# Kernel tuning notes

Hardware: AMD Instinct MI355X
Metric: run time of the kernel (lower is better)

## Reference

```python
import jax, jax.numpy as jnp
import numpy as np

EPS = 0.3
LAYER_NUM = 2
N_NODES = 50000
N_EDGES = 1600000
IN_CH = 256
HIDDEN = 128
OUT_CH = 64


def setup_inputs() -> dict:
    key = jax.random.key(0)
    ks = jax.random.split(key, 8)
    x = jax.random.normal(ks[0], (N_NODES, IN_CH), dtype=jnp.float32)
    edge_index = jax.random.randint(ks[1], (2, N_EDGES), 0, N_NODES, dtype=jnp.int64)
    # xavier-normal-ish scales
    t1_w = jax.random.normal(ks[2], (HIDDEN, IN_CH), dtype=jnp.float32) * (1.414 * (2.0 / (IN_CH + HIDDEN)) ** 0.5)
    t1_b = jnp.zeros((HIDDEN,), dtype=jnp.float32)
    gate_w = jax.random.normal(ks[3], (LAYER_NUM, 2 * HIDDEN), dtype=jnp.float32) * ((2.0 / (2 * HIDDEN + 1)) ** 0.5)
    gate_b = jnp.zeros((LAYER_NUM,), dtype=jnp.float32)
    t2_w = jax.random.normal(ks[4], (OUT_CH, HIDDEN), dtype=jnp.float32) * (1.414 * (2.0 / (HIDDEN + OUT_CH)) ** 0.5)
    t2_b = jnp.zeros((OUT_CH,), dtype=jnp.float32)
    return {"x": x, "edge_index": edge_index, "t1_w": t1_w, "t1_b": t1_b,
            "gate_w": gate_w, "gate_b": gate_b, "t2_w": t2_w, "t2_b": t2_b}


def reference(x, edge_index, t1_w, t1_b, gate_w, gate_b, t2_w, t2_b):
    n = x.shape[0]
    row, col = edge_index[0], edge_index[1]
    # symmetric degree normalization: deg computed over target nodes (row)
    deg = jax.ops.segment_sum(jnp.ones_like(row, dtype=x.dtype), row, num_segments=n)
    dinv = jnp.where(deg > 0, jax.lax.rsqrt(jnp.maximum(deg, 1.0)), 0.0)  # [N]
    edge_norm = dinv[row] * dinv[col]  # [E]

    h = jax.nn.relu(x @ t1_w.T + t1_b)  # [N, H]
    raw = h
    H = h.shape[1]
    for l in range(LAYER_NUM):
        gw_i = gate_w[l, :H]   # weights for h_src (row)
        gw_j = gate_w[l, H:]   # weights for h_dst (col)
        # edge attention g = tanh(gate([h_row || h_col]))  -> [E]
        g = jnp.tanh(h[row] @ gw_i + h[col] @ gw_j + gate_b[l])
        w = g * edge_norm  # [E]
        # scatter-add weighted neighbor features to target nodes
        agg = jax.ops.segment_sum(w[:, None] * h[col], row, num_segments=n)  # [N, H]
        h = EPS * raw + agg
    out = h @ t2_w.T + t2_b  # [N, out]
    return jax.nn.log_softmax(out, axis=1)
```

## Files before the change

### kernel.cpp

```cpp
#include <hip/hip_runtime.h>
#include <math.h>

#define EPSF 0.3f
#define NPB 128
#define SHB 7
#define MAXNB 512
#define CHUNK 4096

typedef __attribute__((ext_vector_type(8))) short bf16x8;
typedef __attribute__((ext_vector_type(4))) float f32x4;

__device__ __forceinline__ uint32_t f2bf(float f) {
    uint32_t u = __float_as_uint(f);
    return (u + 0x7fffu + ((u >> 16) & 1u)) >> 16;
}
__device__ __forceinline__ uint32_t pack2(float lo, float hi) {
    return f2bf(lo) | (f2bf(hi) << 16);
}
__device__ __forceinline__ float bflo(uint32_t u) { return __uint_as_float(u << 16); }
__device__ __forceinline__ float bfhi(uint32_t u) { return __uint_as_float(u & 0xffff0000u); }

__device__ __forceinline__ float fast_tanh(float x) {
    float e = __expf(2.f * x);
    return 1.f - 2.f * __builtin_amdgcn_rcpf(e + 1.f);
}

__device__ __forceinline__ int edge_at(const int* ei, int is64, size_t idx) {
    if (is64) return (int)((const long long*)ei)[idx];
    return ei[idx];
}

__device__ __forceinline__ int detect_is64(const int* ei, int base, int E) {
    __shared__ int s_nz;
    if (threadIdx.x == 0) s_nz = 0;
    __syncthreads();
    int lim = min(512, E - base);
    int nz = 0;
    for (int t = threadIdx.x; t < lim; t += 256)
        nz |= (ei[2 * (size_t)(base + t) + 1] != 0);
    if (nz) atomicOr(&s_nz, 1);
    __syncthreads();
    return s_nz == 0;
}

__global__ __launch_bounds__(256) void k_hist(const int* __restrict__ ei, int E,
                                              int* __restrict__ hist, int nblk, int NB) {
    __shared__ int lh[MAXNB];
    int base = blockIdx.x * CHUNK;
    int is64 = detect_is64(ei, base, E);
    for (int b = threadIdx.x; b < NB; b += 256) lh[b] = 0;
    __syncthreads();
    for (int j = threadIdx.x; j < CHUNK; j += 256) {
        int e = base + j;
        if (e < E) {
            int r = edge_at(ei, is64, e);
            atomicAdd(&lh[r >> SHB], 1);
        }
    }
    __syncthreads();
    for (int b = threadIdx.x; b < NB; b += 256)
        hist[(size_t)b * nblk + blockIdx.x] = lh[b];
}

__global__ void k_scanA(int* __restrict__ hist, int nblk, int* __restrict__ btot) {
    int b = blockIdx.x;
    int lane = threadIdx.x;
    int run = 0;
    for (int seg = 0; seg < nblk; seg += 64) {
        int idx = seg + lane;
        int v = (idx < nblk) ? hist[(size_t)b * nblk + idx] : 0;
        int s = v;
        for (int o = 1; o < 64; o <<= 1) {
            int t = __shfl_up(s, o);
            if (lane >= o) s += t;
        }
        if (idx < nblk) hist[(size_t)b * nblk + idx] = run + s - v;
        run += __shfl(s, 63);
    }
    if (lane == 0) btot[b] = run;
}

__global__ void k_scanB(const int* __restrict__ btot, int NB, int* __restrict__ bbase) {
    __shared__ int s[MAXNB];
    int t = threadIdx.x;
    int v = (t < NB) ? btot[t] : 0;
    s[t] = v;
    __syncthreads();
    for (int o = 1; o < MAXNB; o <<= 1) {
        int x = (t >= o) ? s[t - o] : 0;
        __syncthreads();
        s[t] += x;
        __syncthreads();
    }
    if (t < NB) bbase[t] = s[t] - v;
    if (t == MAXNB - 1) bbase[NB] = s[t];
}

__global__ __launch_bounds__(256) void k_binwrite(const int* __restrict__ ei, int E,
                                                  const int* __restrict__ hist,
                                                  const int* __restrict__ bbase,
                                                  uint32_t* __restrict__ ebuf,
                                                  int nblk, int NB) {
    __shared__ int lcnt[MAXNB];
    int base = blockIdx.x * CHUNK;
    int is64 = detect_is64(ei, base, E);
    for (int b = threadIdx.x; b < NB; b += 256)
        lcnt[b] = bbase[b] + hist[(size_t)b * nblk + blockIdx.x];
    __syncthreads();
    for (int j = threadIdx.x; j < CHUNK; j += 256) {
        int e = base + j;
        if (e < E) {
            int r = edge_at(ei, is64, e);
            int c = edge_at(ei, is64, (size_t)E + e);
            int pos = atomicAdd(&lcnt[r >> SHB], 1);
            ebuf[pos] = (uint32_t)(r & (NPB - 1)) | ((uint32_t)c << SHB);
        }
    }
}

__global__ __launch_bounds__(256) void k_csr(const uint32_t* __restrict__ ebuf,
                                             const int* __restrict__ bbase,
                                             int* __restrict__ rp, float* __restrict__ dinv,
                                             int* __restrict__ ecol, int N, int E, int NB) {
    __shared__ int cnt[NPB];
    __shared__ int sc[NPB];
    __shared__ int cur[NPB];
    int b = blockIdx.x;
    int tid = threadIdx.x;
    int p0 = bbase[b], p1 = bbase[b + 1];
    int n0 = b << SHB;
    if (tid < NPB) cnt[tid] = 0;
    __syncthreads();
    for (int p = p0 + tid; p < p1; p += 256)
        atomicAdd(&cnt[ebuf[p] & (NPB - 1)], 1);
    __syncthreads();
    if (tid < NPB) sc[tid] = cnt[tid];
    __syncthreads();
    for (int o = 1; o < NPB; o <<= 1) {
        int v = (tid < NPB && tid >= o) ? sc[tid - o] : 0;
        __syncthreads();
        if (tid < NPB) sc[tid] += v;
        __syncthreads();
    }
    if (tid < NPB) {
        int off = sc[tid] - cnt[tid];
        cur[tid] = off;
        int node = n0 + tid;
        if (node < N) {
            rp[node] = p0 + off;
            int d = cnt[tid];
            dinv[node] = d > 0 ? rsqrtf((float)d) : 0.f;
        }
    }
    if (b == NB - 1 && tid == 0) rp[N] = E;
    __syncthreads();
    for (int p = p0 + tid; p < p1; p += 256) {
        uint32_t v = ebuf[p];
        int pos = p0 + atomicAdd(&cur[v & (NPB - 1)], 1);
        ecol[pos] = (int)(v >> SHB);
    }
}

__global__ __launch_bounds__(256) void k_gemm1(const float* __restrict__ A,
                                               const float* __restrict__ W,
                                               const float* __restrict__ bias,
                                               uint32_t* __restrict__ hb, int M) {
    __shared__ char As[128 * 128];
    __shared__ char Bs[128 * 128];
    const int tid = threadIdx.x;
    const int lane = tid & 63;
    const int wave = tid >> 6;
    const int wr = wave >> 1, wc = wave & 1;
    const int m0 = blockIdx.x * 128;
    const int lrow = lane & 15, lkg = lane >> 4;
    const int sr = tid >> 3;
    const int sc = (tid & 7) * 8;

    f32x4 acc[4][4];
#pragma unroll
    for (int mi = 0; mi < 4; ++mi)
#pragma unroll
        for (int ni = 0; ni < 4; ++ni) acc[mi][ni] = (f32x4){0.f, 0.f, 0.f, 0.f};

    for (int t = 0; t < 4; ++t) {
        const int k0 = t * 64;
#pragma unroll
        for (int i = 0; i < 4; ++i) {
            int r = i * 32 + sr;
            float4 v0 = make_float4(0.f, 0.f, 0.f, 0.f), v1 = v0;
            if (m0 + r < M) {
                const float* p = &A[(size_t)(m0 + r) * 256 + k0 + sc];
                v0 = *(const float4*)p;
                v1 = *(const float4*)(p + 4);
            }
            uint4 pk = make_uint4(pack2(v0.x, v0.y), pack2(v0.z, v0.w),
                                  pack2(v1.x, v1.y), pack2(v1.z, v1.w));
            uint32_t off = (uint32_t)(r * 128 + sc * 2);
            *(uint4*)(As + (off ^ ((r & 7) << 4))) = pk;
        }
#pragma unroll
        for (int i = 0; i < 4; ++i) {
            int r = i * 32 + sr;
            const float* p = &W[(size_t)r * 256 + k0 + sc];
            float4 v0 = *(const float4*)p;
            float4 v1 = *(const float4*)(p + 4);
            uint4 pk = make_uint4(pack2(v0.x, v0.y), pack2(v0.z, v0.w),
                                  pack2(v1.x, v1.y), pack2(v1.z, v1.w));
            uint32_t off = (uint32_t)(r * 128 + sc * 2);
            *(uint4*)(Bs + (off ^ ((r & 7) << 4))) = pk;
        }
        __syncthreads();
#pragma unroll
        for (int ks = 0; ks < 2; ++ks) {
            bf16x8 af[4], bfr[4];
#pragma unroll
            for (int mi = 0; mi < 4; ++mi) {
                int r = wr * 64 + mi * 16 + lrow;
                uint32_t off = (uint32_t)(r * 128 + ks * 64 + lkg * 16);
                af[mi] = *(const bf16x8*)(As + (off ^ ((r & 7) << 4)));
            }
#pragma unroll
            for (int ni = 0; ni < 4; ++ni) {
                int r = wc * 64 + ni * 16 + lrow;
                uint32_t off = (uint32_t)(r * 128 + ks * 64 + lkg * 16);
                bfr[ni] = *(const bf16x8*)(Bs + (off ^ ((r & 7) << 4)));
            }
#pragma unroll
            for (int mi = 0; mi < 4; ++mi)
#pragma unroll
                for (int ni = 0; ni < 4; ++ni)
                    acc[mi][ni] = __builtin_amdgcn_mfma_f32_16x16x32_bf16(
                        af[mi], bfr[ni], acc[mi][ni], 0, 0, 0);
        }
        __syncthreads();
    }
#pragma unroll
    for (int mi = 0; mi < 4; ++mi) {
#pragma unroll
        for (int ni = 0; ni < 4; ++ni) {
            int n = wc * 64 + ni * 16 + lrow;
            float bv = bias[n];
#pragma unroll
            for (int q = 0; q < 4; ++q) {
                float v = fmaxf(acc[mi][ni][q] + bv, 0.f);
                float vp = __shfl_xor(v, 1);
                int m = m0 + wr * 64 + mi * 16 + lkg * 4 + q;
                if (!(lane & 1) && m < M)
                    hb[(size_t)m * 64 + (n >> 1)] = pack2(v, vp);
            }
        }
    }
}

__global__ __launch_bounds__(256) void k_gemm2(const uint32_t* __restrict__ Abf,
                                               const float* __restrict__ W,
                                               const float* __restrict__ bias,
                                               float* __restrict__ out, int M) {
    __shared__ char As[128 * 128];
    __shared__ char Bs[64 * 128];
    __shared__ float redmax[2][128];
    __shared__ float redsum[2][128];
    const int tid = threadIdx.x;
    const int lane = tid & 63;
    const int wave = tid >> 6;
    const int wr = wave >> 1, wc = wave & 1;
    const int m0 = blockIdx.x * 128;
    const int lrow = lane & 15, lkg = lane >> 4;

    f32x4 acc[4][2];
#pragma unroll
    for (int mi = 0; mi < 4; ++mi)
#pragma unroll
        for (int ni = 0; ni < 2; ++ni) acc[mi][ni] = (f32x4){0.f, 0.f, 0.f, 0.f};

    for (int t = 0; t < 2; ++t) {
#pragma unroll
        for (int i = 0; i < 4; ++i) {
            int r = i * 32 + (tid >> 3);
            uint4 v = make_uint4(0u, 0u, 0u, 0u);
            if (m0 + r < M)
                v = *(const uint4*)&Abf[(size_t)(m0 + r) * 64 + t * 32 + (tid & 7) * 4];
            uint32_t off = (uint32_t)(r * 128 + (tid & 7) * 16);
            *(uint4*)(As + (off ^ ((r & 7) << 4))) = v;
        }
#pragma unroll
        for (int i = 0; i < 2; ++i) {
            int r = i * 32 + (tid >> 3);
            const float* p = &W[(size_t)r * 128 + t * 64 + (tid & 7) * 8];
            float4 v0 = *(const float4*)p, v1 = *(const float4*)(p + 4);
            uint4 pk = make_uint4(pack2(v0.x, v0.y), pack2(v0.z, v0.w),
                                  pack2(v1.x, v1.y), pack2(v1.z, v1.w));
            uint32_t off = (uint32_t)(r * 128 + (tid & 7) * 16);
            *(uint4*)(Bs + (off ^ ((r & 7) << 4))) = pk;
        }
        __syncthreads();
#pragma unroll
        for (int ks = 0; ks < 2; ++ks) {
            bf16x8 af[4], bfr[2];
#pragma unroll
            for (int mi = 0; mi < 4; ++mi) {
                int r = wr * 64 + mi * 16 + lrow;
                uint32_t off = (uint32_t)(r * 128 + ks * 64 + lkg * 16);
                af[mi] = *(const bf16x8*)(As + (off ^ ((r & 7) << 4)));
            }
#pragma unroll
            for (int ni = 0; ni < 2; ++ni) {
                int r = wc * 32 + ni * 16 + lrow;
                uint32_t off = (uint32_t)(r * 128 + ks * 64 + lkg * 16);
                bfr[ni] = *(const bf16x8*)(Bs + (off ^ ((r & 7) << 4)));
            }
#pragma unroll
            for (int mi = 0; mi < 4; ++mi)
#pragma unroll
                for (int ni = 0; ni < 2; ++ni)
                    acc[mi][ni] = __builtin_amdgcn_mfma_f32_16x16x32_bf16(
                        af[mi], bfr[ni], acc[mi][ni], 0, 0, 0);
        }
        __syncthreads();
    }

    float vb[4][2][4];
#pragma unroll
    for (int mi = 0; mi < 4; ++mi)
#pragma unroll
        for (int ni = 0; ni < 2; ++ni) {
            float bv = bias[wc * 32 + ni * 16 + lrow];
#pragma unroll
            for (int q = 0; q < 4; ++q) vb[mi][ni][q] = acc[mi][ni][q] + bv;
        }
#pragma unroll
    for (int mi = 0; mi < 4; ++mi)
#pragma unroll
        for (int q = 0; q < 4; ++q) {
            float mx = fmaxf(vb[mi][0][q], vb[mi][1][q]);
#pragma unroll
            for (int o = 1; o < 16; o <<= 1) mx = fmaxf(mx, __shfl_xor(mx, o));
            if (lrow == 0) redmax[wc][wr * 64 + mi * 16 + lkg * 4 + q] = mx;
        }
    __syncthreads();
    float fmv[4][4];
#pragma unroll
    for (int mi = 0; mi < 4; ++mi)
#pragma unroll
        for (int q = 0; q < 4; ++q) {
            int rl = wr * 64 + mi * 16 + lkg * 4 + q;
            float fm = fmaxf(redmax[0][rl], redmax[1][rl]);
            fmv[mi][q] = fm;
            float e = expf(vb[mi][0][q] - fm) + expf(vb[mi][1][q] - fm);
#pragma unroll
            for (int o = 1; o < 16; o <<= 1) e += __shfl_xor(e, o);
            if (lrow == 0) redsum[wc][rl] = e;
        }
    __syncthreads();
#pragma unroll
    for (int mi = 0; mi < 4; ++mi)
#pragma unroll
        for (int q = 0; q < 4; ++q) {
            int rl = wr * 64 + mi * 16 + lkg * 4 + q;
            int m = m0 + rl;
            if (m < M) {
                float ls = logf(redsum[0][rl] + redsum[1][rl]) + fmv[mi][q];
                out[(size_t)m * 64 + wc * 32 + lrow] = vb[mi][0][q] - ls;
                out[(size_t)m * 64 + wc * 32 + 16 + lrow] = vb[mi][1][q] - ls;
            }
        }
}

__global__ void k_ab(const uint32_t* __restrict__ hbv, const float* __restrict__ gw,
                     const float* __restrict__ gb, int layer,
                     const float* __restrict__ dinv,
                     float* __restrict__ av, float2* __restrict__ bd, int N) {
    int wid = threadIdx.x >> 6, lane = threadIdx.x & 63;
    int i = blockIdx.x * 4 + wid;
    if (i >= N) return;
    uint32_t u = hbv[(size_t)i * 64 + lane];
    float hx = bflo(u), hy = bfhi(u);
    float2 wi = *(const float2*)&gw[lane * 2];
    float2 wj = *(const float2*)&gw[128 + lane * 2];
    float pa = hx * wi.x + hy * wi.y;
    float pb = hx * wj.x + hy * wj.y;
    for (int o = 1; o < 64; o <<= 1) {
        pa += __shfl_xor(pa, o);
        pb += __shfl_xor(pb, o);
    }
    if (lane == 0) {
        av[i] = pa + gb[layer];
        bd[i] = make_float2(pb, dinv[i]);
    }
}

template <bool FUSE_AB, bool RAW_NT>
__global__ __launch_bounds__(256) void k_agg(const uint32_t* __restrict__ hb,
                                             const uint32_t* __restrict__ raw,
                                             const int* __restrict__ rp,
                                             const int* __restrict__ ecol,
                                             const float* __restrict__ av,
                                             const float2* __restrict__ bd,
                                             const float* __restrict__ dinv,
                                             uint32_t* __restrict__ hb_out,
                                             const float* __restrict__ gw_next,
                                             const float* __restrict__ gb_next,
                                             float* __restrict__ av_out,
                                             float2* __restrict__ bd_out, int N) {
    int wid = threadIdx.x >> 6, lane = threadIdx.x & 63;
    int i = blockIdx.x * 4 + wid;
    if (i >= N) return;
    int iu = __builtin_amdgcn_readfirstlane(i);
    int p0 = __builtin_amdgcn_readfirstlane(rp[iu]);
    int p1 = __builtin_amdgcn_readfirstlane(rp[iu + 1]);
    float a_i = av[iu];
    float di = dinv[iu];
    const int lg = lane >> 4;
    const int ll = lane & 15;

    uint32_t r0 = 0, r1 = 0, r2 = 0, r3 = 0;
    if (lane < 16) {
        const uint32_t* rpt = raw + (size_t)i * 64 + ll * 4;
        if (RAW_NT) {
            r0 = __builtin_nontemporal_load(rpt + 0);
            r1 = __builtin_nontemporal_load(rpt + 1);
            r2 = __builtin_nontemporal_load(rpt + 2);
            r3 = __builtin_nontemporal_load(rpt + 3);
        } else {
            r0 = rpt[0]; r1 = rpt[1]; r2 = rpt[2]; r3 = rpt[3];
        }
    }

    float acc[8];
#pragma unroll
    for (int j = 0; j < 8; ++j) acc[j] = 0.f;

    for (int b0 = p0; b0 < p1; b0 += 64) {
        int cnt = min(64, p1 - b0);
        uint32_t wcp = 0u;
        if (lane < cnt) {
            int c = __builtin_nontemporal_load(&ecol[b0 + lane]);
            float2 t = bd[c];
            float w = fast_tanh(a_i + t.x) * t.y;
            wcp = (f2bf(w) << 16) | (uint32_t)c;
        }
        int k = 0;
        for (; k + 8 <= cnt; k += 8) {
            uint32_t wx0 = __builtin_amdgcn_ds_bpermute((k + lg) << 2, (int)wcp);
            uint32_t wx1 = __builtin_amdgcn_ds_bpermute((k + 4 + lg) << 2, (int)wcp);
            float w0 = bfhi(wx0);
            float w1 = bfhi(wx1);
            int c0 = (int)(wx0 & 0xffffu);
            int c1 = (int)(wx1 & 0xffffu);
            uint4 u0 = *((const uint4*)(hb + ((size_t)c0 << 6)) + ll);
            uint4 u1 = *((const uint4*)(hb + ((size_t)c1 << 6)) + ll);
            acc[0] = fmaf(w0, bflo(u0.x), acc[0]); acc[1] = fmaf(w0, bfhi(u0.x), acc[1]);
            acc[2] = fmaf(w0, bflo(u0.y), acc[2]); acc[3] = fmaf(w0, bfhi(u0.y), acc[3]);
            acc[4] = fmaf(w0, bflo(u0.z), acc[4]); acc[5] = fmaf(w0, bfhi(u0.z), acc[5]);
            acc[6] = fmaf(w0, bflo(u0.w), acc[6]); acc[7] = fmaf(w0, bfhi(u0.w), acc[7]);
            acc[0] = fmaf(w1, bflo(u1.x), acc[0]); acc[1] = fmaf(w1, bfhi(u1.x), acc[1]);
            acc[2] = fmaf(w1, bflo(u1.y), acc[2]); acc[3] = fmaf(w1, bfhi(u1.y), acc[3]);
            acc[4] = fmaf(w1, bflo(u1.z), acc[4]); acc[5] = fmaf(w1, bfhi(u1.z), acc[5]);
            acc[6] = fmaf(w1, bflo(u1.w), acc[6]); acc[7] = fmaf(w1, bfhi(u1.w), acc[7]);
        }
        for (; k < cnt; k += 4) {
            uint32_t wx = __builtin_amdgcn_ds_bpermute((k + lg) << 2, (int)wcp);
            float w = bfhi(wx);
            int c = (int)(wx & 0xffffu);
            uint4 u = *((const uint4*)(hb + ((size_t)c << 6)) + ll);
            acc[0] = fmaf(w, bflo(u.x), acc[0]); acc[1] = fmaf(w, bfhi(u.x), acc[1]);
            acc[2] = fmaf(w, bflo(u.y), acc[2]); acc[3] = fmaf(w, bfhi(u.y), acc[3]);
            acc[4] = fmaf(w, bflo(u.z), acc[4]); acc[5] = fmaf(w, bfhi(u.z), acc[5]);
            acc[6] = fmaf(w, bflo(u.w), acc[6]); acc[7] = fmaf(w, bfhi(u.w), acc[7]);
        }
    }
#pragma unroll
    for (int j = 0; j < 8; ++j) {
        acc[j] += __shfl_xor(acc[j], 16);
        acc[j] += __shfl_xor(acc[j], 32);
    }
    if (lane < 16) {
        float o[8];
        o[0] = EPSF * bflo(r0) + di * acc[0]; o[1] = EPSF * bfhi(r0) + di * acc[1];
        o[2] = EPSF * bflo(r1) + di * acc[2]; o[3] = EPSF * bfhi(r1) + di * acc[3];
        o[4] = EPSF * bflo(r2) + di * acc[4]; o[5] = EPSF * bfhi(r2) + di * acc[5];
        o[6] = EPSF * bflo(r3) + di * acc[6]; o[7] = EPSF * bfhi(r3) + di * acc[7];
        uint4 w4;
        w4.x = pack2(o[0], o[1]); w4.y = pack2(o[2], o[3]);
        w4.z = pack2(o[4], o[5]); w4.w = pack2(o[6], o[7]);
        *((uint4*)(hb_out + (size_t)i * 64) + ll) = w4;
        if (FUSE_AB) {
            float pa = 0.f, pb = 0.f;
#pragma unroll
            for (int j = 0; j < 8; ++j) {
                int ch = ll * 8 + j;
                pa = fmaf(o[j], gw_next[ch], pa);
                pb = fmaf(o[j], gw_next[128 + ch], pb);
            }
#pragma unroll
            for (int off = 1; off < 16; off <<= 1) {
                pa += __shfl_xor(pa, off);
                pb += __shfl_xor(pb, off);
            }
            if (ll == 0) {
                av_out[i] = pa + gb_next[0];
                bd_out[i] = make_float2(pb, di);
            }
        }
    }
}

extern "C" void kernel_launch(void* const* d_in, const int* in_sizes, int n_in,
                              void* d_out, int out_size, void* d_ws, size_t ws_size,
                              hipStream_t stream) {
    const float* x = (const float*)d_in[0];
    const int* ei = (const int*)d_in[1];
    const float* t1w = (const float*)d_in[2];
    const float* t1b = (const float*)d_in[3];
    const float* gw = (const float*)d_in[4];
    const float* gb = (const float*)d_in[5];
    const float* t2w = (const float*)d_in[6];
    const float* t2b = (const float*)d_in[7];
    float* out = (float*)d_out;

    const int INC = 256;
    const int N = in_sizes[0] / INC;
    const int E = in_sizes[1] / 2;
    const int NB = (N + NPB - 1) >> SHB;
    const int nblk = (E + CHUNK - 1) / CHUNK;

    char* ws = (char*)d_ws;
    auto alloc = [&](size_t bytes) {
        char* p = ws;
        ws += (bytes + 255) & ~(size_t)255;
        return p;
    };
    int* hist = (int*)alloc((size_t)NB * nblk * 4);
    int* btot = (int*)alloc((size_t)NB * 4);
    int* bbase = (int*)alloc((size_t)(NB + 1) * 4);
    uint32_t* ebuf = (uint32_t*)alloc((size_t)E * 4);
    int* rp = (int*)alloc((size_t)(N + 1) * 4);
    float* dinv = (float*)alloc((size_t)N * 4);
    int* ecol = (int*)alloc((size_t)E * 4);
    float* av0 = (float*)alloc((size_t)N * 4);
    float* av1 = (float*)alloc((size_t)N * 4);
    float2* bd0 = (float2*)alloc((size_t)N * 8);
    float2* bd1 = (float2*)alloc((size_t)N * 8);
    uint32_t* hb0 = (uint32_t*)alloc((size_t)N * 64 * 4);
    uint32_t* hb1 = (uint32_t*)alloc((size_t)N * 64 * 4);
    uint32_t* hb2 = (uint32_t*)alloc((size_t)N * 64 * 4);

    k_hist<<<nblk, 256, 0, stream>>>(ei, E, hist, nblk, NB);
    k_scanA<<<NB, 64, 0, stream>>>(hist, nblk, btot);
    k_scanB<<<1, MAXNB, 0, stream>>>(btot, NB, bbase);
    k_binwrite<<<nblk, 256, 0, stream>>>(ei, E, hist, bbase, ebuf, nblk, NB);
    k_csr<<<NB, 256, 0, stream>>>(ebuf, bbase, rp, dinv, ecol, N, E, NB);

    k_gemm1<<<(N + 127) / 128, 256, 0, stream>>>(x, t1w, t1b, hb0, N);

    k_ab<<<(N + 3) / 4, 256, 0, stream>>>(hb0, gw + 0 * 256, gb, 0, dinv, av0, bd0, N);
    k_agg<true, false><<<(N + 3) / 4, 256, 0, stream>>>(
        hb0, hb0, rp, ecol, av0, bd0, dinv, hb1, gw + 1 * 256, gb + 1, av1, bd1, N);
    k_agg<false, true><<<(N + 3) / 4, 256, 0, stream>>>(
        hb1, hb0, rp, ecol, av1, bd1, dinv, hb2, nullptr, nullptr, nullptr, nullptr, N);

    k_gemm2<<<(N + 127) / 128, 256, 0, stream>>>(hb2, t2w, t2b, out, N);
}
```

Before: 205.1 us.

## Bin edges by row block and column range to improve gather locality

The counting-sort key becomes (row block, column bucket of 8192 nodes) instead of row block alone, so edges inside each CSR row block end up grouped by source-column range. This aims to make the later neighbor feature gathers more cache-local. In exchange the histogram grows (NB*NCB keys per chunk, about 2.3k with the default sizes), scanA becomes a serial per-key loop over chunks, and scanB becomes a single-block multi-pass scan. Both add preprocessing cost.

Measured after the change: 313.1 us. 1.53x slower.

```diff
diff --git a/kernel.cpp b/kernel.cpp
--- a/kernel.cpp
+++ b/kernel.cpp
@@ -4,7 +4,8 @@
 #define EPSF 0.3f
 #define NPB 128
 #define SHB 7
-#define MAXNB 512
+#define CBSH 13
+#define MAXK 4096
 #define CHUNK 4096
 
 typedef __attribute__((ext_vector_type(8))) short bf16x8;
@@ -44,75 +45,82 @@
 }
 
 __global__ __launch_bounds__(256) void k_hist(const int* __restrict__ ei, int E,
-                                              int* __restrict__ hist, int nblk, int NB) {
-    __shared__ int lh[MAXNB];
+                                              int* __restrict__ hist, int nkeys, int NCB) {
+    __shared__ int lh[MAXK];
     int base = blockIdx.x * CHUNK;
     int is64 = detect_is64(ei, base, E);
-    for (int b = threadIdx.x; b < NB; b += 256) lh[b] = 0;
-    __syncthreads();
-    for (int j = threadIdx.x; j < CHUNK; j += 256) {
-        int e = base + j;
-        if (e < E) {
-            int r = edge_at(ei, is64, e);
-            atomicAdd(&lh[r >> SHB], 1);
-        }
-    }
-    __syncthreads();
-    for (int b = threadIdx.x; b < NB; b += 256)
-        hist[(size_t)b * nblk + blockIdx.x] = lh[b];
-}
-
-__global__ void k_scanA(int* __restrict__ hist, int nblk, int* __restrict__ btot) {
-    int b = blockIdx.x;
-    int lane = threadIdx.x;
-    int run = 0;
-    for (int seg = 0; seg < nblk; seg += 64) {
-        int idx = seg + lane;
-        int v = (idx < nblk) ? hist[(size_t)b * nblk + idx] : 0;
-        int s = v;
-        for (int o = 1; o < 64; o <<= 1) {
-            int t = __shfl_up(s, o);
-            if (lane >= o) s += t;
-        }
-        if (idx < nblk) hist[(size_t)b * nblk + idx] = run + s - v;
-        run += __shfl(s, 63);
-    }
-    if (lane == 0) btot[b] = run;
-}
-
-__global__ void k_scanB(const int* __restrict__ btot, int NB, int* __restrict__ bbase) {
-    __shared__ int s[MAXNB];
-    int t = threadIdx.x;
-    int v = (t < NB) ? btot[t] : 0;
-    s[t] = v;
-    __syncthreads();
-    for (int o = 1; o < MAXNB; o <<= 1) {
-        int x = (t >= o) ? s[t - o] : 0;
-        __syncthreads();
-        s[t] += x;
-        __syncthreads();
-    }
-    if (t < NB) bbase[t] = s[t] - v;
-    if (t == MAXNB - 1) bbase[NB] = s[t];
-}
-
-__global__ __launch_bounds__(256) void k_binwrite(const int* __restrict__ ei, int E,
-                                                  const int* __restrict__ hist,
-                                                  const int* __restrict__ bbase,
-                                                  uint32_t* __restrict__ ebuf,
-                                                  int nblk, int NB) {
-    __shared__ int lcnt[MAXNB];
-    int base = blockIdx.x * CHUNK;
-    int is64 = detect_is64(ei, base, E);
-    for (int b = threadIdx.x; b < NB; b += 256)
-        lcnt[b] = bbase[b] + hist[(size_t)b * nblk + blockIdx.x];
+    for (int b = threadIdx.x; b < nkeys; b += 256) lh[b] = 0;
     __syncthreads();
     for (int j = threadIdx.x; j < CHUNK; j += 256) {
         int e = base + j;
         if (e < E) {
             int r = edge_at(ei, is64, e);
             int c = edge_at(ei, is64, (size_t)E + e);
-            int pos = atomicAdd(&lcnt[r >> SHB], 1);
+            atomicAdd(&lh[(r >> SHB) * NCB + (c >> CBSH)], 1);
+        }
+    }
+    __syncthreads();
+    int* hrow = hist + (size_t)blockIdx.x * nkeys;
+    for (int b = threadIdx.x; b < nkeys; b += 256) hrow[b] = lh[b];
+}
+
+__global__ void k_scanA(int* __restrict__ hist, int nblk, int nkeys,
+                        int* __restrict__ btot) {
+    int key = blockIdx.x * 64 + threadIdx.x;
+    if (key >= nkeys) return;
+    int run = 0;
+    for (int blk = 0; blk < nblk; ++blk) {
+        size_t idx = (size_t)blk * nkeys + key;
+        int v = hist[idx];
+        hist[idx] = run;
+        run += v;
+    }
+    btot[key] = run;
+}
+
+__global__ void k_scanB(const int* __restrict__ btot, int n, int* __restrict__ bbase) {
+    __shared__ int s[256];
+    __shared__ int carry;
+    if (threadIdx.x == 0) carry = 0;
+    __syncthreads();
+    for (int base = 0; base < n; base += 256) {
+        int idx = base + threadIdx.x;
+        int v = (idx < n) ? btot[idx] : 0;
+        s[threadIdx.x] = v;
+        __syncthreads();
+        for (int o = 1; o < 256; o <<= 1) {
+            int x = (threadIdx.x >= o) ? s[threadIdx.x - o] : 0;
+            __syncthreads();
+            s[threadIdx.x] += x;
+            __syncthreads();
+        }
+        if (idx < n) bbase[idx] = carry + s[threadIdx.x] - v;
+        int tot = s[255];
+        __syncthreads();
+        if (threadIdx.x == 0) carry += tot;
+        __syncthreads();
+    }
+    if (threadIdx.x == 0) bbase[n] = carry;
+}
+
+__global__ __launch_bounds__(256) void k_binwrite(const int* __restrict__ ei, int E,
+                                                  const int* __restrict__ hist,
+                                                  const int* __restrict__ bbase,
+                                                  uint32_t* __restrict__ ebuf,
+                                                  int nkeys, int NCB) {
+    __shared__ int lcnt[MAXK];
+    int base = blockIdx.x * CHUNK;
+    int is64 = detect_is64(ei, base, E);
+    const int* hrow = hist + (size_t)blockIdx.x * nkeys;
+    for (int b = threadIdx.x; b < nkeys; b += 256)
+        lcnt[b] = bbase[b] + hrow[b];
+    __syncthreads();
+    for (int j = threadIdx.x; j < CHUNK; j += 256) {
+        int e = base + j;
+        if (e < E) {
+            int r = edge_at(ei, is64, e);
+            int c = edge_at(ei, is64, (size_t)E + e);
+            int pos = atomicAdd(&lcnt[(r >> SHB) * NCB + (c >> CBSH)], 1);
             ebuf[pos] = (uint32_t)(r & (NPB - 1)) | ((uint32_t)c << SHB);
         }
     }
@@ -121,13 +129,14 @@
 __global__ __launch_bounds__(256) void k_csr(const uint32_t* __restrict__ ebuf,
                                              const int* __restrict__ bbase,
                                              int* __restrict__ rp, float* __restrict__ dinv,
-                                             int* __restrict__ ecol, int N, int E, int NB) {
+                                             int* __restrict__ ecol, int N, int E,
+                                             int NB, int NCB) {
     __shared__ int cnt[NPB];
     __shared__ int sc[NPB];
     __shared__ int cur[NPB];
     int b = blockIdx.x;
     int tid = threadIdx.x;
-    int p0 = bbase[b], p1 = bbase[b + 1];
+    int p0 = bbase[b * NCB], p1 = bbase[b * NCB + NCB];
     int n0 = b << SHB;
     if (tid < NPB) cnt[tid] = 0;
     __syncthreads();
@@ -522,6 +531,8 @@
     const int N = in_sizes[0] / INC;
     const int E = in_sizes[1] / 2;
     const int NB = (N + NPB - 1) >> SHB;
+    const int NCB = ((N - 1) >> CBSH) + 1;
+    const int nkeys = NB * NCB;
     const int nblk = (E + CHUNK - 1) / CHUNK;
 
     char* ws = (char*)d_ws;
@@ -530,9 +541,9 @@
         ws += (bytes + 255) & ~(size_t)255;
         return p;
     };
-    int* hist = (int*)alloc((size_t)NB * nblk * 4);
-    int* btot = (int*)alloc((size_t)NB * 4);
-    int* bbase = (int*)alloc((size_t)(NB + 1) * 4);
+    int* hist = (int*)alloc((size_t)nkeys * nblk * 4);
+    int* btot = (int*)alloc((size_t)nkeys * 4);
+    int* bbase = (int*)alloc((size_t)(nkeys + 1) * 4);
     uint32_t* ebuf = (uint32_t*)alloc((size_t)E * 4);
     int* rp = (int*)alloc((size_t)(N + 1) * 4);
     float* dinv = (float*)alloc((size_t)N * 4);
@@ -545,11 +556,11 @@
     uint32_t* hb1 = (uint32_t*)alloc((size_t)N * 64 * 4);
     uint32_t* hb2 = (uint32_t*)alloc((size_t)N * 64 * 4);
 
-    k_hist<<<nblk, 256, 0, stream>>>(ei, E, hist, nblk, NB);
-    k_scanA<<<NB, 64, 0, stream>>>(hist, nblk, btot);
-    k_scanB<<<1, MAXNB, 0, stream>>>(btot, NB, bbase);
-    k_binwrite<<<nblk, 256, 0, stream>>>(ei, E, hist, bbase, ebuf, nblk, NB);
-    k_csr<<<NB, 256, 0, stream>>>(ebuf, bbase, rp, dinv, ecol, N, E, NB);
+    k_hist<<<nblk, 256, 0, stream>>>(ei, E, hist, nkeys, NCB);
+    k_scanA<<<(nkeys + 63) / 64, 64, 0, stream>>>(hist, nblk, nkeys, btot);
+    k_scanB<<<1, 256, 0, stream>>>(btot, nkeys, bbase);
+    k_binwrite<<<nblk, 256, 0, stream>>>(ei, E, hist, bbase, ebuf, nkeys, NCB);
+    k_csr<<<NB, 256, 0, stream>>>(ebuf, bbase, rp, dinv, ecol, N, E, NB, NCB);
 
     k_gemm1<<<(N + 127) / 128, 256, 0, stream>>>(x, t1w, t1b, hb0, N);
 
```
